# Performance work log

Hardware: AMD Instinct MI355X
Metric: run time of the kernel (lower is better)

Reference implementation:

```python
import jax, jax.numpy as jnp
import numpy as np


def setup_inputs() -> dict:
    key = jax.random.key(0)
    k1, k2 = jax.random.split(key)
    B, H, W, E = 8, 32, 32, 256   # latent grid (NHWC layout, as in vector_quantize)
    N_E = 16384                   # codebook size
    x = jax.random.normal(k1, (B, H, W, E), dtype=jnp.float32)
    codebook = jax.random.normal(k2, (N_E, E), dtype=jnp.float32)
    return {"x": x, "codebook": codebook}


def reference(x, codebook):
    # d[b,h,w,k] = ||x[b,h,w] - codebook[k]||^2 (expanded form, as in source)
    x_sq = jnp.sum(x * x, axis=-1, keepdims=True)            # [B,H,W,1]
    cb_sq = jnp.sum(codebook * codebook, axis=1)              # [N_E]
    cross = jnp.einsum('bhwe,ke->bhwk', x, codebook)          # [B,H,W,N_E]
    d = x_sq + cb_sq - 2.0 * cross
    indices = jnp.argmin(d, axis=-1)                          # [B,H,W]
    x_q = jnp.take(codebook, indices, axis=0)                 # one-hot @ codebook == row gather
    # straight-through / ReplaceGrad: forward value is x_q, gradient flows to x
    return x + jax.lax.stop_gradient(x_q - x)
```

## Files before the change

### kernel.cpp

```cpp
#include <hip/hip_runtime.h>
#include <stdint.h>

#define M_PIX 8192
#define N_CB  16384
#define KD    256

typedef float f32x4 __attribute__((ext_vector_type(4)));
typedef int   i32x4 __attribute__((ext_vector_type(4)));
typedef int   i32x8 __attribute__((ext_vector_type(8)));
typedef unsigned long long ull;

#define OFF_CF8  (0ULL)
#define OFF_XF8  (4ULL << 20)
#define OFF_CBSQ (6ULL << 20)
#define OFF_SLOT (7ULL << 20)
#define WS_REQ   (15ULL << 20)

__device__ __forceinline__ unsigned int fkey(float s) {
  unsigned int f = __float_as_uint(s);
  return f ^ ((unsigned int)(((int)f) >> 31) | 0x80000000u);
}
__device__ __forceinline__ unsigned char f2e4m3(float v) {
  float av = fminf(fabsf(v), 448.0f);
  const unsigned s = (__float_as_uint(v) >> 24) & 0x80u;
  unsigned m;
  if (av >= 0.015625f) {
    unsigned u = __float_as_uint(av);
    u += 0x7FFFFu + ((u >> 20) & 1u);
    m = (((u >> 23) - 120u) << 3) | ((u >> 20) & 7u);
  } else {
    m = (unsigned)(int)rintf(av * 512.0f);
  }
  return (unsigned char)(s | m);
}
__device__ __forceinline__ void gl_lds16(const unsigned char* g, char* l) {
  __builtin_amdgcn_global_load_lds(
      (const __attribute__((address_space(1))) unsigned int*)(const void*)g,
      (__attribute__((address_space(3))) unsigned int*)(void*)l,
      16, 0, 0);
}
__device__ __forceinline__ void ins2f(float k, float& v1, float& v2) {
  v2 = fminf(v2, fmaxf(v1, k));
  v1 = fminf(v1, k);
}
__device__ __forceinline__ void merge2(float p, float q, float& v1, float& v2) {
  const float M = fmaxf(v1, p);
  v1 = fminf(v1, p);
  v2 = fminf(fminf(v2, q), M);
}
__device__ __forceinline__ i32x8 ld32(const char* p, int addr) {
  const i32x4 lo = *(const i32x4*)(const void*)(p + addr);
  const i32x4 hi = *(const i32x4*)(const void*)(p + (addr ^ 16));
  return (i32x8){lo.x, lo.y, lo.z, lo.w, hi.x, hi.y, hi.z, hi.w};
}

__global__ __launch_bounds__(256) void prep_kernel(
    const float* __restrict__ x, const float* __restrict__ cb,
    unsigned char* __restrict__ Cf8, unsigned char* __restrict__ Xf8,
    float* __restrict__ cbsq) {
  const int wid = threadIdx.x >> 6, lane = threadIdx.x & 63;
  const int row = blockIdx.x * 4 + wid;
  const bool isCb = (row < N_CB);
  const int rowL = isCb ? row : row - N_CB;
  const float* src = (isCb ? cb : x) + (size_t)rowL * KD;
  const float4 v = ((const float4*)src)[lane];
  uchar4 pk;
  pk.x = f2e4m3(v.x); pk.y = f2e4m3(v.y); pk.z = f2e4m3(v.z); pk.w = f2e4m3(v.w);
  *(uchar4*)(void*)((isCb ? Cf8 : Xf8) + (size_t)rowL * KD + lane * 4) = pk;
  if (isCb) {
    float ss = v.x*v.x + v.y*v.y + v.z*v.z + v.w*v.w;
    #pragma unroll
    for (int off = 32; off > 0; off >>= 1) ss += __shfl_xor(ss, off);
    if (lane == 0) cbsq[rowL] = ss;
  }
}


__global__ __launch_bounds__(256, 3) void gemm_top2_kernel(
    const unsigned char* __restrict__ Xf8, const unsigned char* __restrict__ Cf8,
    const float* __restrict__ cbsq, float2* __restrict__ slots) {
  __shared__ __align__(16) char smem[36864];
  char* A_s = smem;
  char* B_s = smem + 16384;
  float* v1p = (float*)smem;
  float* v2p = (float*)(smem + 18432);

  const int tid = threadIdx.x;
  const int wid = tid >> 6, lane = tid & 63;
  const int wy = wid >> 1, wx = wid & 1;
  const int q = lane >> 4, c = lane & 15;

  const int bx = blockIdx.x & 7, bg = blockIdx.x >> 3;
  const int mt = bg >> 4;
  const int nt = bx * 16 + (bg & 15);
  const int m0 = mt * 128, n0 = nt * 128;

  const int swz = (c & 7) << 4;
  int aaddr[4], baddr[4];
  #pragma unroll
  for (int i = 0; i < 4; i++) {
    aaddr[i] = (((wy * 64 + i * 16 + c) * 128) + q * 32) ^ swz;
    baddr[i] = ((((wx * 64 + i * 16 + c) * 128) + q * 32) ^ swz) + 16384;
  }

  const f32x4 zf = {0.f, 0.f, 0.f, 0.f};
  f32x4 acc[4][4];
  #pragma unroll
  for (int i = 0; i < 4; i++)
    #pragma unroll
    for (int j = 0; j < 4; j++) acc[i][j] = zf;

  const int srow8 = lane >> 3;
  const int sgb = ((lane & 7) ^ srow8) * 16;

  #pragma unroll
  for (int j = 0; j < 4; j++) {
    const int chunk = j * 4 + wid;
    const int row = chunk * 8 + srow8;
    gl_lds16(Xf8 + (size_t)(m0 + row) * KD + sgb, A_s + chunk * 1024);
    gl_lds16(Cf8 + (size_t)(n0 + row) * KD + sgb, B_s + chunk * 1024);
  }
  __syncthreads();

  i32x8 af0[4], bf0[4];
  #pragma unroll
  for (int mi = 0; mi < 4; mi++) af0[mi] = ld32(smem, aaddr[mi]);
  #pragma unroll
  for (int ni = 0; ni < 4; ni++) bf0[ni] = ld32(smem, baddr[ni]);
  __builtin_amdgcn_sched_barrier(0);
  __syncthreads();

  #pragma unroll
  for (int j = 0; j < 4; j++) {
    const int chunk = j * 4 + wid;
    const int row = chunk * 8 + srow8;
    gl_lds16(Xf8 + (size_t)(m0 + row) * KD + sgb + 128, A_s + chunk * 1024);
    gl_lds16(Cf8 + (size_t)(n0 + row) * KD + sgb + 128, B_s + chunk * 1024);
  }
  __builtin_amdgcn_sched_barrier(0);

  #pragma unroll
  for (int mi = 0; mi < 4; mi++)
    #pragma unroll
    for (int ni = 0; ni < 4; ni++)
      acc[mi][ni] = __builtin_amdgcn_mfma_scale_f32_16x16x128_f8f6f4(
          af0[mi], bf0[ni], acc[mi][ni], 0, 0,
          0, 0x7F7F7F7F,
          0, 0x7F7F7F7F);
  __builtin_amdgcn_sched_barrier(0);
  __syncthreads();

  float cs[4]; unsigned colp[4];
  #pragma unroll
  for (int ni = 0; ni < 4; ni++) {
    colp[ni] = wx * 64 + ni * 16 + c;
    cs[ni] = cbsq[n0 + colp[ni]];
  }

  #pragma unroll
  for (int mi = 0; mi < 4; mi++) af0[mi] = ld32(smem, aaddr[mi]);
  #pragma unroll
  for (int ni = 0; ni < 4; ni++) bf0[ni] = ld32(smem, baddr[ni]);
  __builtin_amdgcn_sched_barrier(0);
  __syncthreads();

  #pragma unroll
  for (int mi = 0; mi < 4; mi++)
    #pragma unroll
    for (int ni = 0; ni < 4; ni++)
      acc[mi][ni] = __builtin_amdgcn_mfma_scale_f32_16x16x128_f8f6f4(
          af0[mi], bf0[ni], acc[mi][ni], 0, 0,
          0, 0x7F7F7F7F, 0, 0x7F7F7F7F);

  const float FINF = __uint_as_float(0x7F800000u);

  #pragma unroll
  for (int mi = 0; mi < 4; mi++) {
    #pragma unroll
    for (int r = 0; r < 4; r++) {
      float k[4];
      #pragma unroll
      for (int ni = 0; ni < 4; ni++) {
        const float s = fmaf(-2.f, acc[mi][ni][r], cs[ni]);
        k[ni] = __uint_as_float((__float_as_uint(s) & 0xFFFFFF80u) | colp[ni]);
      }
      const float m1 = fminf(k[0], k[1]), M1 = fmaxf(k[0], k[1]);
      const float m2 = fminf(k[2], k[3]), M2 = fmaxf(k[2], k[3]);
      const float v1 = fminf(m1, m2);
      const float v2 = fminf(fmaxf(m1, m2), fminf(M1, M2));
      const int row = wy * 64 + mi * 16 + q * 4 + r;
      const int slot = wx * 16 + c;
      v1p[row * 36 + slot] = v1;
      v2p[row * 36 + slot] = v2;
    }
  }
  __syncthreads();

  {
    const int srow = tid >> 1, half = tid & 1;
    float v1 = FINF, v2 = FINF;
    #pragma unroll
    for (int jj = 0; jj < 4; jj++) {
      const float4 a = *(const float4*)(const void*)(v1p + srow * 36 + half * 16 + jj * 4);
      const float4 b = *(const float4*)(const void*)(v2p + srow * 36 + half * 16 + jj * 4);
      merge2(a.x, b.x, v1, v2);
      merge2(a.y, b.y, v1, v2);
      merge2(a.z, b.z, v1, v2);
      merge2(a.w, b.w, v1, v2);
    }
    const float b1 = __shfl_xor(v1, 1), b2 = __shfl_xor(v2, 1);
    const float hi = fmaxf(v1, b1);
    v1 = fminf(v1, b1);
    v2 = fminf(fminf(v2, b2), hi);
    if (!half)
      slots[(size_t)nt * M_PIX + m0 + srow] = make_float2(v1, v2);
  }
}

__global__ __launch_bounds__(256) void reduce_rescore_gather(
    const float* __restrict__ x, const float* __restrict__ cb,
    const float* __restrict__ cbsq, const float2* __restrict__ slots,
    float* __restrict__ out) {
  const int wid = threadIdx.x >> 6, lane = threadIdx.x & 63;
  const int pixel = blockIdx.x * 4 + wid;

  const float2 sA = slots[(size_t)lane * M_PIX + pixel];
  const float2 sB = slots[(size_t)(64 + lane) * M_PIX + pixel];
  const float sc[4] = {sA.x, sA.y, sB.x, sB.y};
  float mn = fminf(fminf(sc[0], sc[1]), fminf(sc[2], sc[3]));
  #pragma unroll
  for (int off = 1; off < 64; off <<= 1) mn = fminf(mn, __shfl_xor(mn, off));
  const float thr = mn + 10.0f;

  const float4 xv = ((const float4*)x)[(size_t)pixel * 64 + lane];
  ull best = ~0ULL;
  #pragma unroll
  for (int j = 0; j < 4; j++) {
    ull mask = __ballot(sc[j] < thr);
    while (mask) {
      const int src = (int)__ffsll((long long)mask) - 1;
      mask &= mask - 1;
      const float val = __shfl(sc[j], src);
      const unsigned ij = (unsigned)(((j >> 1) * 64 + src) * 128) +
                          (__float_as_uint(val) & 127u);
      const float4 cv = ((const float4*)cb)[(size_t)ij * 64 + lane];
      float d = xv.x*cv.x + xv.y*cv.y + xv.z*cv.z + xv.w*cv.w;
      #pragma unroll
      for (int off = 1; off < 64; off <<= 1) d += __shfl_xor(d, off);
      const float sv = fmaf(-2.f, d, cbsq[ij]);
      const ull k = ((ull)fkey(sv) << 32) | ij;
      best = k < best ? k : best;
    }
  }
  const unsigned w = (unsigned)best;
  ((float4*)out)[(size_t)pixel * 64 + lane] = ((const float4*)cb)[(size_t)w * 64 + lane];
}

__global__ __launch_bounds__(256) void fallback_kernel(
    const float* __restrict__ x, const float* __restrict__ cb,
    float* __restrict__ out) {
  __shared__ float xs[256];
  __shared__ unsigned long long keys[4];
  __shared__ int widx;
  const int p = blockIdx.x;
  const int tid = threadIdx.x, wid = tid >> 6, lane = tid & 63;
  xs[tid] = x[(size_t)p * KD + tid];
  __syncthreads();
  const float4 xv = ((const float4*)xs)[lane];
  float bestS = 3.4e38f; int bestI = 0;
  for (int k = wid; k < N_CB; k += 4) {
    const float4 cv = ((const float4*)cb)[(size_t)k * 64 + lane];
    float t = cv.x*(cv.x - 2.f*xv.x) + cv.y*(cv.y - 2.f*xv.y)
            + cv.z*(cv.z - 2.f*xv.z) + cv.w*(cv.w - 2.f*xv.w);
    #pragma unroll
    for (int off = 1; off < 64; off <<= 1) t += __shfl_xor(t, off);
    if (t < bestS) { bestS = t; bestI = k; }
  }
  if (lane == 0)
    keys[wid] = ((unsigned long long)fkey(bestS) << 32) | (unsigned int)bestI;
  __syncthreads();
  if (tid == 0) {
    unsigned long long m = keys[0];
    for (int i = 1; i < 4; i++) if (keys[i] < m) m = keys[i];
    widx = (int)(unsigned int)(m & 0xFFFFFFFFULL);
  }
  __syncthreads();
  out[(size_t)p * KD + tid] = cb[(size_t)widx * KD + tid];
}

extern "C" void kernel_launch(void* const* d_in, const int* in_sizes, int n_in,
                              void* d_out, int out_size, void* d_ws, size_t ws_size,
                              hipStream_t stream) {
  const float* x  = (const float*)d_in[0];
  const float* cb = (const float*)d_in[1];
  float* out = (float*)d_out;

  if (ws_size < WS_REQ) {
    fallback_kernel<<<M_PIX, 256, 0, stream>>>(x, cb, out);
    return;
  }

  char* ws = (char*)d_ws;
  unsigned char* Cf8 = (unsigned char*)(ws + OFF_CF8);
  unsigned char* Xf8 = (unsigned char*)(ws + OFF_XF8);
  float* cbsq        = (float*)(ws + OFF_CBSQ);
  float2* slots      = (float2*)(ws + OFF_SLOT);

  prep_kernel<<<(N_CB + M_PIX) / 4, 256, 0, stream>>>(x, cb, Cf8, Xf8, cbsq);
  gemm_top2_kernel<<<M_PIX, 256, 0, stream>>>(Xf8, Cf8, cbsq, slots);
  reduce_rescore_gather<<<M_PIX / 4, 256, 0, stream>>>(x, cb, cbsq, slots, out);
}
```

Before: 139.5 us.

## Restructure rescore kernel to batch candidates per 64-pixel block via shared list

The reduce/rescore/gather kernel now handles 64 pixels per block instead of one pixel per wavefront. It loads the slot table coalesced into shared memory, computes per-pixel thresholds, and compacts surviving candidates into a shared list with an atomic counter. Each candidate is then rescored by a 16-lane group instead of a full 64-lane wave, with the best result kept via atomicMin. This targets the serial ballot loop, the wide 64-lane reductions and the uncoalesced slot reads. The costs are shared-memory atomics, a fallback path that rescores serially in a single thread when more than 512 candidates survive, and only 128 blocks in the grid.

```diff
diff --git a/kernel.cpp b/kernel.cpp
--- a/kernel.cpp
+++ b/kernel.cpp
@@ -38,10 +38,6 @@
       (const __attribute__((address_space(1))) unsigned int*)(const void*)g,
       (__attribute__((address_space(3))) unsigned int*)(void*)l,
       16, 0, 0);
-}
-__device__ __forceinline__ void ins2f(float k, float& v1, float& v2) {
-  v2 = fminf(v2, fmaxf(v1, k));
-  v1 = fminf(v1, k);
 }
 __device__ __forceinline__ void merge2(float p, float q, float& v1, float& v2) {
   const float M = fmaxf(v1, p);
@@ -221,39 +217,87 @@
     const float* __restrict__ x, const float* __restrict__ cb,
     const float* __restrict__ cbsq, const float2* __restrict__ slots,
     float* __restrict__ out) {
-  const int wid = threadIdx.x >> 6, lane = threadIdx.x & 63;
-  const int pixel = blockIdx.x * 4 + wid;
-
-  const float2 sA = slots[(size_t)lane * M_PIX + pixel];
-  const float2 sB = slots[(size_t)(64 + lane) * M_PIX + pixel];
-  const float sc[4] = {sA.x, sA.y, sB.x, sB.y};
-  float mn = fminf(fminf(sc[0], sc[1]), fminf(sc[2], sc[3]));
-  #pragma unroll
-  for (int off = 1; off < 64; off <<= 1) mn = fminf(mn, __shfl_xor(mn, off));
-  const float thr = mn + 10.0f;
-
-  const float4 xv = ((const float4*)x)[(size_t)pixel * 64 + lane];
-  ull best = ~0ULL;
-  #pragma unroll
-  for (int j = 0; j < 4; j++) {
-    ull mask = __ballot(sc[j] < thr);
-    while (mask) {
-      const int src = (int)__ffsll((long long)mask) - 1;
-      mask &= mask - 1;
-      const float val = __shfl(sc[j], src);
-      const unsigned ij = (unsigned)(((j >> 1) * 64 + src) * 128) +
-                          (__float_as_uint(val) & 127u);
-      const float4 cv = ((const float4*)cb)[(size_t)ij * 64 + lane];
-      float d = xv.x*cv.x + xv.y*cv.y + xv.z*cv.z + xv.w*cv.w;
-      #pragma unroll
-      for (int off = 1; off < 64; off <<= 1) d += __shfl_xor(d, off);
-      const float sv = fmaf(-2.f, d, cbsq[ij]);
-      const ull k = ((ull)fkey(sv) << 32) | ij;
-      best = k < best ? k : best;
+  __shared__ float2 sT[128][64];
+  __shared__ float pmin[4][64];
+  __shared__ ull bestk[64];
+  __shared__ unsigned cnt;
+  __shared__ uint2 cl[512];
+
+  const int tid = threadIdx.x;
+  const int w = tid >> 6, lane = tid & 63;
+  const int P0 = blockIdx.x * 64;
+
+  if (tid < 64) bestk[tid] = ~0ULL;
+  if (tid == 0) cnt = 0;
+
+  #pragma unroll
+  for (int i = 0; i < 32; i++) {
+    const int t = w * 32 + i;
+    sT[t][lane] = slots[(size_t)t * M_PIX + P0 + lane];
+  }
+  __syncthreads();
+
+  float mnp = __uint_as_float(0x7F800000u);
+  #pragma unroll
+  for (int i = 0; i < 32; i++)
+    mnp = fminf(mnp, sT[w * 32 + i][lane].x);
+  pmin[w][lane] = mnp;
+  __syncthreads();
+  const float thr = fminf(fminf(pmin[0][lane], pmin[1][lane]),
+                          fminf(pmin[2][lane], pmin[3][lane])) + 10.0f;
+
+  for (int i = 0; i < 32; i++) {
+    const int t = w * 32 + i;
+    const float2 v = sT[t][lane];
+    #pragma unroll
+    for (int s = 0; s < 2; s++) {
+      const float sv = s ? v.y : v.x;
+      if (sv < thr) {
+        const unsigned ij = (unsigned)t * 128u + (__float_as_uint(sv) & 127u);
+        const unsigned idx = atomicAdd(&cnt, 1u);
+        if (idx < 512u) {
+          cl[idx] = make_uint2((unsigned)lane, ij);
+        } else {
+          const float* xr = x + (size_t)(P0 + lane) * KD;
+          const float* cr = cb + (size_t)ij * KD;
+          float d = 0.f;
+          for (int e = 0; e < KD; e++) d = fmaf(xr[e], cr[e], d);
+          atomicMin(&bestk[lane],
+                    ((ull)fkey(fmaf(-2.f, d, cbsq[ij])) << 32) | ij);
+        }
+      }
     }
   }
-  const unsigned w = (unsigned)best;
-  ((float4*)out)[(size_t)pixel * 64 + lane] = ((const float4*)cb)[(size_t)w * 64 + lane];
+  __syncthreads();
+
+  const int g = tid >> 4, lg = tid & 15;
+  const unsigned n = cnt < 512u ? cnt : 512u;
+  for (unsigned e = (unsigned)g; e < n; e += 16u) {
+    const uint2 ent = cl[e];
+    const unsigned p = ent.x, ij = ent.y;
+    float d = 0.f;
+    #pragma unroll
+    for (int k = 0; k < 4; k++) {
+      const float4 xv = ((const float4*)x)[(size_t)(P0 + p) * 64 + lg * 4 + k];
+      const float4 cv = ((const float4*)cb)[(size_t)ij * 64 + lg * 4 + k];
+      d += xv.x*cv.x + xv.y*cv.y + xv.z*cv.z + xv.w*cv.w;
+    }
+    #pragma unroll
+    for (int off = 1; off < 16; off <<= 1) d += __shfl_xor(d, off);
+    const float sv = fmaf(-2.f, d, cbsq[ij]);
+    if (lg == 0) atomicMin(&bestk[p], ((ull)fkey(sv) << 32) | ij);
+  }
+  __syncthreads();
+
+  #pragma unroll
+  for (int k4 = 0; k4 < 4; k4++) {
+    const int pp = g * 4 + k4;
+    const unsigned wj = (unsigned)bestk[pp];
+    #pragma unroll
+    for (int k = 0; k < 4; k++)
+      ((float4*)out)[(size_t)(P0 + pp) * 64 + lg * 4 + k] =
+          ((const float4*)cb)[(size_t)wj * 64 + lg * 4 + k];
+  }
 }
 
 __global__ __launch_bounds__(256) void fallback_kernel(
@@ -308,5 +352,5 @@
 
   prep_kernel<<<(N_CB + M_PIX) / 4, 256, 0, stream>>>(x, cb, Cf8, Xf8, cbsq);
   gemm_top2_kernel<<<M_PIX, 256, 0, stream>>>(Xf8, Cf8, cbsq, slots);
-  reduce_rescore_gather<<<M_PIX / 4, 256, 0, stream>>>(x, cb, cbsq, slots, out);
-}
+  reduce_rescore_gather<<<M_PIX / 64, 256, 0, stream>>>(x, cb, cbsq, slots, out);
+}
```

Result: slower. 145.8 us (+4.6%).
